# Kernel tuning notes

Measured on AMD Instinct MI355X. Metric: run time of the kernel, lower is better.

## Reference

```python
import jax, jax.numpy as jnp
import numpy as np

MARGIN = 0.25
SCALE = 64.0
OP = 1.0 + MARGIN
ON = -MARGIN
DELTA_P = 1.0 - MARGIN
DELTA_N = MARGIN
NEG_FILL = -1e4  # effectively -inf for these logits (|logit| < ~300)

B, D = 8192, 1024
N_IDS = 512


def setup_inputs() -> dict:
    key = jax.random.key(0)
    k1, k2 = jax.random.split(key)
    inputs = jax.random.normal(k1, (B, D), dtype=jnp.float32)
    targets = jax.random.randint(k2, (B,), 0, N_IDS, dtype=jnp.int64)
    return {"inputs": inputs, "targets": targets}


def reference(inputs, targets):
    # L2-normalize embeddings (torch F.normalize uses eps=1e-12 clamp on norm)
    norm = jnp.maximum(jnp.linalg.norm(inputs, axis=1, keepdims=True), 1e-12)
    x = inputs / norm
    sim = x @ x.T  # [B, B] cosine similarities

    same = targets[:, None] == targets[None, :]
    eye = jnp.eye(targets.shape[0], dtype=bool)
    pos_mask = same & ~eye
    neg_mask = ~same

    sim_sg = jax.lax.stop_gradient(sim)  # .detach() in original
    ap = jnp.maximum(OP - sim_sg, 0.0)
    an = jnp.maximum(sim_sg - ON, 0.0)

    logit_p = -ap * (sim - DELTA_P) * SCALE
    logit_n = an * (sim - DELTA_N) * SCALE

    lse_p = jax.nn.logsumexp(jnp.where(pos_mask, logit_p, NEG_FILL), axis=1)
    lse_n = jax.nn.logsumexp(jnp.where(neg_mask, logit_n, NEG_FILL), axis=1)

    loss_i = jax.nn.softplus(lse_n + lse_p)  # [B]
    valid = pos_mask.any(axis=1) & neg_mask.any(axis=1)

    total = jnp.sum(jnp.where(valid, loss_i, 0.0))
    count = jnp.maximum(jnp.sum(valid), 1)
    return total / count
```

## Files before the change

kernel.cpp:

```cpp
#include <hip/hip_runtime.h>
#include <hip/hip_bf16.h>
#include <math.h>

#define THREADS 256
typedef unsigned short ushortT;
typedef __attribute__((ext_vector_type(8))) short bf16x8;
typedef __attribute__((ext_vector_type(4))) float f32x4;

__device__ __forceinline__ void async16(const ushortT* g, ushortT* l) {
  __builtin_amdgcn_global_load_lds(
      (const __attribute__((address_space(1))) unsigned int*)g,
      (__attribute__((address_space(3))) unsigned int*)l, 16, 0, 0);
}

__device__ __forceinline__ ushortT f2bf(float f) {
  __hip_bfloat16 h = __float2bfloat16(f);
  return *reinterpret_cast<ushortT*>(&h);
}

__global__ __launch_bounds__(THREADS) void k_prep(const float* __restrict__ x,
                                                  ushortT* __restrict__ xn, int D) {
  __shared__ float red[4];
  const int row = blockIdx.x;
  const int tid = threadIdx.x;
  const int gid = row * (D / 4) + tid;
  const float4 v = reinterpret_cast<const float4*>(x)[gid];
  float s = v.x * v.x + v.y * v.y + v.z * v.z + v.w * v.w;
  #pragma unroll
  for (int off = 32; off; off >>= 1) s += __shfl_xor(s, off);
  if ((tid & 63) == 0) red[tid >> 6] = s;
  __syncthreads();
  const float tot = red[0] + red[1] + red[2] + red[3];
  const float rn = 1.0f / fmaxf(sqrtf(tot), 1e-12f);
  ushort4 o;
  o.x = f2bf(v.x * rn); o.y = f2bf(v.y * rn);
  o.z = f2bf(v.z * rn); o.w = f2bf(v.w * rn);
  reinterpret_cast<ushort4*>(xn)[gid] = o;
}

__global__ __launch_bounds__(THREADS, 2) void k_main_mfma(const ushortT* __restrict__ xn,
                                                          const int* __restrict__ tgt,
                                                          float4* __restrict__ partial,
                                                          int D, int nb) {
  __shared__ ushortT Asm[128 * 32];
  __shared__ ushortT Bsm[128 * 32];

  const int tid = threadIdx.x;
  const int lane = tid & 63;
  const int w = tid >> 6;

  const int b = blockIdx.x;
  int bi = (int)((2.f * nb + 1.f -
                  sqrtf((2.f * nb + 1.f) * (2.f * nb + 1.f) - 8.f * (float)b)) * 0.5f);
  while ((bi + 1) * (2 * nb - bi) / 2 <= b) ++bi;
  while (bi * (2 * nb - bi + 1) / 2 > b) --bi;
  const int bj = bi + (b - bi * (2 * nb - bi + 1) / 2);
  const bool isdiag = (bi == bj);

  const int i0 = bi * 128, j0 = bj * 128;
  const int wr = (w >> 1) * 64, wc = (w & 1) * 64;

  const int sr = lane & 15, sc = lane >> 4;
  const ushortT* gA0 = xn + (size_t)(i0 + w * 16 + sr) * D + sc * 8;
  const ushortT* gA1 = gA0 + (size_t)64 * D;
  const ushortT* gB0 = xn + (size_t)(j0 + w * 16 + sr) * D + sc * 8;
  const ushortT* gB1 = gB0 + (size_t)64 * D;
  ushortT* lA0 = &Asm[w * 512];
  ushortT* lA1 = &Asm[(w + 4) * 512];
  ushortT* lB0 = &Bsm[w * 512];
  ushortT* lB1 = &Bsm[(w + 4) * 512];

  const ushortT* Bbase = isdiag ? Asm : Bsm;
  const int aoff = ((w >> 1) * 4) * 512 + lane * 8;
  const int boff = ((w & 1) * 4) * 512 + lane * 8;

  f32x4 acc[4][4];
  #pragma unroll
  for (int mt = 0; mt < 4; ++mt)
    #pragma unroll
    for (int nt = 0; nt < 4; ++nt)
      acc[mt][nt] = (f32x4){0.f, 0.f, 0.f, 0.f};

  const int kiters = D / 32;
  for (int kk = 0; kk < kiters; ++kk) {
    const size_t ko = (size_t)kk * 32;
    async16(gA0 + ko, lA0);
    async16(gA1 + ko, lA1);
    if (!isdiag) {
      async16(gB0 + ko, lB0);
      async16(gB1 + ko, lB1);
    }
    __syncthreads();
    bf16x8 afr[4], bfr[4];
    #pragma unroll
    for (int mt = 0; mt < 4; ++mt)
      afr[mt] = *reinterpret_cast<const bf16x8*>(&Asm[aoff + mt * 512]);
    #pragma unroll
    for (int nt = 0; nt < 4; ++nt)
      bfr[nt] = *reinterpret_cast<const bf16x8*>(&Bbase[boff + nt * 512]);
    #pragma unroll
    for (int mt = 0; mt < 4; ++mt)
      #pragma unroll
      for (int nt = 0; nt < 4; ++nt)
        acc[mt][nt] = __builtin_amdgcn_mfma_f32_16x16x32_bf16(afr[mt], bfr[nt], acc[mt][nt], 0, 0, 0);
    __syncthreads();
  }

  const int q = lane >> 4, c = lane & 15;
  int tj[4];
  #pragma unroll
  for (int nt = 0; nt < 4; ++nt) tj[nt] = tgt[j0 + wc + nt * 16 + c];
  int tir[16];
  #pragma unroll
  for (int mt = 0; mt < 4; ++mt) {
    const int4 t4 = *reinterpret_cast<const int4*>(tgt + i0 + wr + mt * 16 + q * 4);
    tir[mt * 4 + 0] = t4.x; tir[mt * 4 + 1] = t4.y;
    tir[mt * 4 + 2] = t4.z; tir[mt * 4 + 3] = t4.w;
  }

  #pragma unroll
  for (int mt = 0; mt < 4; ++mt) {
    #pragma unroll
    for (int reg = 0; reg < 4; ++reg) {
      const int i = i0 + wr + mt * 16 + q * 4 + reg;
      const int ti = tir[mt * 4 + reg];
      float m = -1e30f, sn = 0.f;
      float sel[4];
      #pragma unroll
      for (int nt = 0; nt < 4; ++nt) {
        const float s = acc[mt][nt][reg];
        const int j = j0 + wc + nt * 16 + c;
        const bool same = (tj[nt] == ti);
        const bool vpos = same && (j != i);
        const float lp = (fminf(s, 1.25f) - 1.25f) * fmaf(s, 64.f, -48.f);
        const float sv = vpos ? lp : -2e30f;
        sel[nt] = sv;
        m = fmaxf(m, sv);
        const float ln = (fmaxf(s, -0.25f) + 0.25f) * fmaf(s, 64.f, -16.f);
        const float en = __expf(ln);
        sn += same ? 0.f : en;
      }
      #pragma unroll
      for (int off = 1; off < 16; off <<= 1) m = fmaxf(m, __shfl_xor(m, off));
      float sp = 0.f;
      #pragma unroll
      for (int nt = 0; nt < 4; ++nt) sp += __expf(sel[nt] - m);
      #pragma unroll
      for (int off = 1; off < 16; off <<= 1) {
        sp += __shfl_xor(sp, off);
        sn += __shfl_xor(sn, off);
      }
      if (c == 0) {
        float4 o; o.x = m; o.y = sp; o.z = 0.f; o.w = sn;
        partial[((size_t)i * nb + bj) * 2 + (w & 1)] = o;
      }
    }
  }

  if (!isdiag) {
    #pragma unroll
    for (int nt = 0; nt < 4; ++nt) {
      const int jt = tj[nt];
      const int jrow = j0 + wc + nt * 16 + c;
      float m = -1e30f, sn = 0.f;
      float sel[16];
      #pragma unroll
      for (int mt = 0; mt < 4; ++mt) {
        #pragma unroll
        for (int reg = 0; reg < 4; ++reg) {
          const float s = acc[mt][nt][reg];
          const bool same = (tir[mt * 4 + reg] == jt);
          const float lp = (fminf(s, 1.25f) - 1.25f) * fmaf(s, 64.f, -48.f);
          const float sv = same ? lp : -2e30f;
          sel[mt * 4 + reg] = sv;
          m = fmaxf(m, sv);
          const float ln = (fmaxf(s, -0.25f) + 0.25f) * fmaf(s, 64.f, -16.f);
          const float en = __expf(ln);
          sn += same ? 0.f : en;
        }
      }
      m = fmaxf(m, __shfl_xor(m, 16));
      m = fmaxf(m, __shfl_xor(m, 32));
      float sp = 0.f;
      #pragma unroll
      for (int k = 0; k < 16; ++k) sp += __expf(sel[k] - m);
      sp += __shfl_xor(sp, 16); sp += __shfl_xor(sp, 32);
      sn += __shfl_xor(sn, 16); sn += __shfl_xor(sn, 32);
      if (lane < 16) {
        float4 o; o.x = m; o.y = sp; o.z = 0.f; o.w = sn;
        partial[((size_t)jrow * nb + bi) * 2 + (w >> 1)] = o;
      }
    }
  }
}

__global__ __launch_bounds__(THREADS) void k_reduce(const float4* __restrict__ partial,
                                                    float* __restrict__ row_loss) {
  const int lane = threadIdx.x & 63;
  const int row = blockIdx.x * 4 + (threadIdx.x >> 6);
  const float4 a = partial[(size_t)row * 128 + lane];
  const float4 b = partial[(size_t)row * 128 + 64 + lane];
  float mp = fmaxf(a.x, b.x);
  float sp = a.y * __expf(a.x - mp) + b.y * __expf(b.x - mp);
  float sn = a.w + b.w;
  #pragma unroll
  for (int off = 1; off < 64; off <<= 1) {
    const float m2 = __shfl_xor(mp, off), s2 = __shfl_xor(sp, off);
    const float nm = fmaxf(mp, m2);
    sp = sp * __expf(mp - nm) + s2 * __expf(m2 - nm);
    mp = nm;
    sn += __shfl_xor(sn, off);
  }
  if (lane == 0) {
    float loss = -1.0f;
    if (sp > 0.f && sn > 0.f) {
      const float z = mp + logf(sp) + logf(sn);
      loss = (z > 0.f) ? (z + log1pf(__expf(-z))) : log1pf(__expf(z));
    }
    row_loss[row] = loss;
  }
}

__global__ __launch_bounds__(THREADS) void k_final(const float* __restrict__ row_loss,
                                                   float* __restrict__ out, int B) {
  __shared__ float ssum[4];
  __shared__ float scnt[4];
  const int tid = threadIdx.x;
  float sum = 0.f, cnt = 0.f;
  for (int i = tid; i < B; i += THREADS) {
    const float l = row_loss[i];
    if (l >= 0.f) { sum += l; cnt += 1.f; }
  }
  #pragma unroll
  for (int off = 32; off; off >>= 1) {
    sum += __shfl_xor(sum, off);
    cnt += __shfl_xor(cnt, off);
  }
  if ((tid & 63) == 0) { ssum[tid >> 6] = sum; scnt[tid >> 6] = cnt; }
  __syncthreads();
  if (tid == 0) {
    float ts = 0.f, tc = 0.f;
    #pragma unroll
    for (int w = 0; w < 4; ++w) { ts += ssum[w]; tc += scnt[w]; }
    out[0] = ts / fmaxf(tc, 1.f);
  }
}

extern "C" void kernel_launch(void* const* d_in, const int* in_sizes, int n_in,
                              void* d_out, int out_size, void* d_ws, size_t ws_size,
                              hipStream_t stream) {
  const float* x = (const float*)d_in[0];
  const int* tgt = (const int*)d_in[1];
  float* out = (float*)d_out;
  const int B = in_sizes[1];
  const int D = in_sizes[0] / B;
  const int nb = B / 128;

  ushortT* xn = (ushortT*)d_ws;
  float4* partial = (float4*)((char*)d_ws + (size_t)B * D * 2);
  float* row_loss = (float*)((char*)d_ws + (size_t)B * D * 2 + (size_t)B * 2 * nb * 16);

  k_prep<<<B, THREADS, 0, stream>>>(x, xn, D);
  k_main_mfma<<<nb * (nb + 1) / 2, THREADS, 0, stream>>>(xn, tgt, partial, D, nb);
  k_reduce<<<B / 4, THREADS, 0, stream>>>(partial, row_loss);
  k_final<<<1, THREADS, 0, stream>>>(row_loss, out, B);
}
```

Measured before the change: 250.9 us.

## Raise main kernel occupancy to 4 blocks/CU by trimming register pressure

Changes launch bounds from 2 to 4 blocks per CU on the MFMA tile kernel and reduces live registers to fit. The B fragments are now loaded two at a time instead of all four. Global addresses use 32-bit offsets from a base pointer, and the transposed epilogue recomputes the positive logits rather than keeping a 16-element array. The aim is more waves per CU to hide the synchronous LDS load and barrier latency, at the risk of spills or extra ALU from recomputation.

```diff
diff --git a/kernel.cpp b/kernel.cpp
--- a/kernel.cpp
+++ b/kernel.cpp
@@ -38,7 +38,7 @@
   reinterpret_cast<ushort4*>(xn)[gid] = o;
 }
 
-__global__ __launch_bounds__(THREADS, 2) void k_main_mfma(const ushortT* __restrict__ xn,
+__global__ __launch_bounds__(THREADS, 4) void k_main_mfma(const ushortT* __restrict__ xn,
                                                           const int* __restrict__ tgt,
                                                           float4* __restrict__ partial,
                                                           int D, int nb) {
@@ -61,10 +61,10 @@
   const int wr = (w >> 1) * 64, wc = (w & 1) * 64;
 
   const int sr = lane & 15, sc = lane >> 4;
-  const ushortT* gA0 = xn + (size_t)(i0 + w * 16 + sr) * D + sc * 8;
-  const ushortT* gA1 = gA0 + (size_t)64 * D;
-  const ushortT* gB0 = xn + (size_t)(j0 + w * 16 + sr) * D + sc * 8;
-  const ushortT* gB1 = gB0 + (size_t)64 * D;
+  const ushortT* baseA = xn + (size_t)i0 * D;
+  const ushortT* baseB = xn + (size_t)j0 * D;
+  const int offA = (w * 16 + sr) * D + sc * 8;
+  const int hstep = 64 * D;
   ushortT* lA0 = &Asm[w * 512];
   ushortT* lA1 = &Asm[(w + 4) * 512];
   ushortT* lB0 = &Bsm[w * 512];
@@ -83,26 +83,36 @@
 
   const int kiters = D / 32;
   for (int kk = 0; kk < kiters; ++kk) {
-    const size_t ko = (size_t)kk * 32;
-    async16(gA0 + ko, lA0);
-    async16(gA1 + ko, lA1);
+    const int ko = kk * 32;
+    async16(baseA + offA + ko, lA0);
+    async16(baseA + offA + hstep + ko, lA1);
     if (!isdiag) {
-      async16(gB0 + ko, lB0);
-      async16(gB1 + ko, lB1);
+      async16(baseB + offA + ko, lB0);
+      async16(baseB + offA + hstep + ko, lB1);
     }
     __syncthreads();
-    bf16x8 afr[4], bfr[4];
+    bf16x8 afr[4];
     #pragma unroll
     for (int mt = 0; mt < 4; ++mt)
       afr[mt] = *reinterpret_cast<const bf16x8*>(&Asm[aoff + mt * 512]);
-    #pragma unroll
-    for (int nt = 0; nt < 4; ++nt)
-      bfr[nt] = *reinterpret_cast<const bf16x8*>(&Bbase[boff + nt * 512]);
-    #pragma unroll
-    for (int mt = 0; mt < 4; ++mt)
-      #pragma unroll
-      for (int nt = 0; nt < 4; ++nt)
-        acc[mt][nt] = __builtin_amdgcn_mfma_f32_16x16x32_bf16(afr[mt], bfr[nt], acc[mt][nt], 0, 0, 0);
+    {
+      bf16x8 b0 = *reinterpret_cast<const bf16x8*>(&Bbase[boff]);
+      bf16x8 b1 = *reinterpret_cast<const bf16x8*>(&Bbase[boff + 512]);
+      #pragma unroll
+      for (int mt = 0; mt < 4; ++mt)
+        acc[mt][0] = __builtin_amdgcn_mfma_f32_16x16x32_bf16(afr[mt], b0, acc[mt][0], 0, 0, 0);
+      #pragma unroll
+      for (int mt = 0; mt < 4; ++mt)
+        acc[mt][1] = __builtin_amdgcn_mfma_f32_16x16x32_bf16(afr[mt], b1, acc[mt][1], 0, 0, 0);
+      b0 = *reinterpret_cast<const bf16x8*>(&Bbase[boff + 2 * 512]);
+      b1 = *reinterpret_cast<const bf16x8*>(&Bbase[boff + 3 * 512]);
+      #pragma unroll
+      for (int mt = 0; mt < 4; ++mt)
+        acc[mt][2] = __builtin_amdgcn_mfma_f32_16x16x32_bf16(afr[mt], b0, acc[mt][2], 0, 0, 0);
+      #pragma unroll
+      for (int mt = 0; mt < 4; ++mt)
+        acc[mt][3] = __builtin_amdgcn_mfma_f32_16x16x32_bf16(afr[mt], b1, acc[mt][3], 0, 0, 0);
+    }
     __syncthreads();
   }
 
@@ -163,7 +173,6 @@
       const int jt = tj[nt];
       const int jrow = j0 + wc + nt * 16 + c;
       float m = -1e30f, sn = 0.f;
-      float sel[16];
       #pragma unroll
       for (int mt = 0; mt < 4; ++mt) {
         #pragma unroll
@@ -171,9 +180,7 @@
           const float s = acc[mt][nt][reg];
           const bool same = (tir[mt * 4 + reg] == jt);
           const float lp = (fminf(s, 1.25f) - 1.25f) * fmaf(s, 64.f, -48.f);
-          const float sv = same ? lp : -2e30f;
-          sel[mt * 4 + reg] = sv;
-          m = fmaxf(m, sv);
+          m = fmaxf(m, same ? lp : -2e30f);
           const float ln = (fmaxf(s, -0.25f) + 0.25f) * fmaf(s, 64.f, -16.f);
           const float en = __expf(ln);
           sn += same ? 0.f : en;
@@ -183,7 +190,15 @@
       m = fmaxf(m, __shfl_xor(m, 32));
       float sp = 0.f;
       #pragma unroll
-      for (int k = 0; k < 16; ++k) sp += __expf(sel[k] - m);
+      for (int mt = 0; mt < 4; ++mt) {
+        #pragma unroll
+        for (int reg = 0; reg < 4; ++reg) {
+          const float s = acc[mt][nt][reg];
+          const bool same = (tir[mt * 4 + reg] == jt);
+          const float lp = (fminf(s, 1.25f) - 1.25f) * fmaf(s, 64.f, -48.f);
+          sp += __expf((same ? lp : -2e30f) - m);
+        }
+      }
       sp += __shfl_xor(sp, 16); sp += __shfl_xor(sp, 32);
       sn += __shfl_xor(sn, 16); sn += __shfl_xor(sn, 32);
       if (lane < 16) {
```

After: 261.5 us. 4.2% more time.
